# Kernel tuning notes

Measured on AMD Instinct MI355X. Metric: run time of the kernel, lower is better.

The kernel has to match this reference:

```python
import jax, jax.numpy as jnp
import numpy as np

B, S, D, H = 4, 2048, 1024, 16
DK = D // H  # d_k = d_v = 64


def setup_inputs() -> dict:
    key = jax.random.key(0)
    ks = jax.random.split(key, 9)
    sc = 0.02
    return {
        "x": jax.random.normal(ks[0], (B, S, D), dtype=jnp.float32),
        "Wq": jax.random.normal(ks[1], (H, D, DK), dtype=jnp.float32) * sc,
        "bq": jax.random.normal(ks[2], (H, DK), dtype=jnp.float32) * sc,
        "Wk": jax.random.normal(ks[3], (H, D, DK), dtype=jnp.float32) * sc,
        "bk": jax.random.normal(ks[4], (H, DK), dtype=jnp.float32) * sc,
        "Wv": jax.random.normal(ks[5], (H, D, DK), dtype=jnp.float32) * sc,
        "bv": jax.random.normal(ks[6], (H, DK), dtype=jnp.float32) * sc,
        "Wo": jax.random.normal(ks[7], (D, D), dtype=jnp.float32) * sc,
        "bo": jax.random.normal(ks[8], (D,), dtype=jnp.float32) * sc,
    }


def reference(x, Wq, bq, Wk, bk, Wv, bv, Wo, bo):
    # per-head learned projections (heads stacked on leading axis h)
    Q = jnp.einsum("bsd,hdk->bhsk", x, Wq) + bq[None, :, None, :]
    K = jnp.einsum("bsd,hdk->bhsk", x, Wk) + bk[None, :, None, :]
    V = jnp.einsum("bsd,hdk->bhsk", x, Wv) + bv[None, :, None, :]
    scores = jnp.einsum("bhsk,bhtk->bhst", Q, K) / jnp.sqrt(jnp.float32(DK))
    # causal mask: future_sight=0, past_sight=None -> positions t > s replaced by -1e9
    s_idx = jnp.arange(S)
    causal = s_idx[:, None] >= s_idx[None, :]  # [S, S] True where allowed
    scores = jnp.where(causal[None, None, :, :], scores, jnp.float32(-1e9))
    attn = jax.nn.softmax(scores, axis=-1)
    out = jnp.einsum("bhst,bhtk->bhsk", attn, V)  # [B, H, S, DK]
    # concat heads along feature dim (head order matches ModuleList order)
    cat = out.transpose(0, 2, 1, 3).reshape(B, S, D)
    return cat @ Wo + bo
```

## Files before the change

kernel.cpp:

```cpp
#include <hip/hip_runtime.h>
#include <stdint.h>

#define B_  4
#define S_  2048
#define D_  1024
#define H_  16
#define DK_ 64
#define M_  (B_ * S_)

typedef __attribute__((ext_vector_type(8))) short bf16x8;
typedef __attribute__((ext_vector_type(4))) float f32x4;

#define QSCALE 0.1803368801111204f

__device__ __forceinline__ uint16_t f2bf(float f) {
    uint32_t u = __builtin_bit_cast(uint32_t, f);
    u = (u + 0x7FFFu + ((u >> 16) & 1u)) >> 16;
    return (uint16_t)u;
}

__device__ __forceinline__ uint32_t pk2bf(float hi, float lo) {
    uint32_t a = __builtin_bit_cast(uint32_t, hi) + 0x8000u;
    uint32_t b = __builtin_bit_cast(uint32_t, lo) + 0x8000u;
    return __builtin_amdgcn_perm(a, b, 0x07060302u);
}

__global__ __launch_bounds__(256) void cvt_bf16_kernel(const float* __restrict__ in,
                                                       uint16_t* __restrict__ out, int n) {
    int i = (blockIdx.x * 256 + threadIdx.x) * 8;
    if (i >= n) return;
    float4 a = *(const float4*)&in[i];
    float4 b = *(const float4*)&in[i + 4];
    uint16_t o[8] = {f2bf(a.x), f2bf(a.y), f2bf(a.z), f2bf(a.w),
                     f2bf(b.x), f2bf(b.y), f2bf(b.z), f2bf(b.w)};
    *(uint4*)&out[i] = *(const uint4*)o;
}

__global__ __launch_bounds__(256) void transpose_cvt_kernel(
    const float* __restrict__ in, uint16_t* __restrict__ out, int R, int C) {
    __shared__ __align__(16) uint16_t tile[64][72];
    const int mat = blockIdx.z;
    const float* inm = in + (size_t)mat * R * C;
    uint16_t* outm = out + (size_t)mat * R * C;
    const int r0 = blockIdx.x * 64, c0 = blockIdx.y * 64;
    const int t = threadIdx.x;
    const int lr = t >> 2, lc = (t & 3) * 16;
    uint16_t tmp[16];
    #pragma unroll
    for (int j = 0; j < 16; j += 4) {
        float4 v = *(const float4*)&inm[(size_t)(r0 + lr) * C + c0 + lc + j];
        tmp[j] = f2bf(v.x); tmp[j + 1] = f2bf(v.y); tmp[j + 2] = f2bf(v.z); tmp[j + 3] = f2bf(v.w);
    }
    *(uint4*)&tile[lr][lc]     = ((const uint4*)tmp)[0];
    *(uint4*)&tile[lr][lc + 8] = ((const uint4*)tmp)[1];
    __syncthreads();
    const int oc = t >> 2, orr = (t & 3) * 16;
    uint16_t ot[16];
    #pragma unroll
    for (int j = 0; j < 16; ++j) ot[j] = tile[orr + j][oc];
    *(uint4*)&outm[(size_t)(c0 + oc) * R + r0 + orr]     = ((const uint4*)ot)[0];
    *(uint4*)&outm[(size_t)(c0 + oc) * R + r0 + orr + 8] = ((const uint4*)ot)[1];
}

__global__ __launch_bounds__(256) void qkv_mfma_kernel(
    const uint16_t* __restrict__ xb, const uint16_t* __restrict__ Wt,
    const float* __restrict__ bq, const float* __restrict__ bk, const float* __restrict__ bv,
    uint16_t* __restrict__ Q, uint16_t* __restrict__ K, uint16_t* __restrict__ V)
{
    __shared__ __align__(16) uint16_t As[128][72];
    __shared__ __align__(16) uint16_t Bs[128][72];
    const int tid = threadIdx.x;
    const int nb = blockIdx.x;
    const int sel = nb >> 3, npair = nb & 7;
    const int m0 = blockIdx.y * 128;
    const int lane = tid & 63, w = tid >> 6;
    const int wr = w >> 1, wc = w & 1;
    const int ll = lane & 15, quad = lane >> 4;

    const uint16_t* Bg = Wt + (size_t)nb * 128 * 1024;
    const float* bias = (sel == 0) ? bq : (sel == 1) ? bk : bv;

    const int ar = tid >> 1, ac = (tid & 1) * 32;

    f32x4 acc[4][4];
    const f32x4 zz = {0.f, 0.f, 0.f, 0.f};
    #pragma unroll
    for (int i = 0; i < 4; ++i)
        #pragma unroll
        for (int j = 0; j < 4; ++j) acc[i][j] = zz;

    for (int k0 = 0; k0 < 1024; k0 += 64) {
        __syncthreads();
        const uint16_t* ag = &xb[(size_t)(m0 + ar) * 1024 + k0 + ac];
        uint4 a0 = *(const uint4*)(ag);
        uint4 a1 = *(const uint4*)(ag + 8);
        uint4 a2 = *(const uint4*)(ag + 16);
        uint4 a3 = *(const uint4*)(ag + 24);
        const uint16_t* bg = &Bg[(size_t)ar * 1024 + k0 + ac];
        uint4 b0 = *(const uint4*)(bg);
        uint4 b1 = *(const uint4*)(bg + 8);
        uint4 b2 = *(const uint4*)(bg + 16);
        uint4 b3 = *(const uint4*)(bg + 24);
        *(uint4*)&As[ar][ac]      = a0;
        *(uint4*)&As[ar][ac + 8]  = a1;
        *(uint4*)&As[ar][ac + 16] = a2;
        *(uint4*)&As[ar][ac + 24] = a3;
        *(uint4*)&Bs[ar][ac]      = b0;
        *(uint4*)&Bs[ar][ac + 8]  = b1;
        *(uint4*)&Bs[ar][ac + 16] = b2;
        *(uint4*)&Bs[ar][ac + 24] = b3;
        __syncthreads();
        #pragma unroll
        for (int ks = 0; ks < 2; ++ks) {
            bf16x8 af[4], bfv[4];
            #pragma unroll
            for (int mt = 0; mt < 4; ++mt)
                af[mt] = *(const bf16x8*)&As[wr * 64 + mt * 16 + ll][ks * 32 + quad * 8];
            #pragma unroll
            for (int nt = 0; nt < 4; ++nt)
                bfv[nt] = *(const bf16x8*)&Bs[wc * 64 + nt * 16 + ll][ks * 32 + quad * 8];
            #pragma unroll
            for (int mt = 0; mt < 4; ++mt)
                #pragma unroll
                for (int nt = 0; nt < 4; ++nt)
                    acc[mt][nt] = __builtin_amdgcn_mfma_f32_16x16x32_bf16(af[mt], bfv[nt], acc[mt][nt], 0, 0, 0);
        }
    }

    if (sel == 2) {
        #pragma unroll
        for (int nt = 0; nt < 4; ++nt) {
            const int nl = wc * 64 + nt * 16 + ll;
            const int hh = npair * 2 + (nl >> 6);
            const int dk = nl & 63;
            const float bval = bias[npair * 128 + nl];
            #pragma unroll
            for (int mt = 0; mt < 4; ++mt) {
                int m = m0 + wr * 64 + mt * 16 + quad * 4;
                int b = m >> 11, s = m & 2047;
                uint2 pv;
                pv.x = pk2bf(acc[mt][nt][1] + bval, acc[mt][nt][0] + bval);
                pv.y = pk2bf(acc[mt][nt][3] + bval, acc[mt][nt][2] + bval);
                *(uint2*)&V[((size_t)(b * 16 + hh) * 64 + dk) * 2048 + s] = pv;
            }
        }
    } else {
        uint16_t* Out = (sel == 0) ? Q : K;
        const float qs = (sel == 0) ? QSCALE : 1.0f;
        #pragma unroll
        for (int nt = 0; nt < 4; ++nt) {
            const int nl = wc * 64 + nt * 16 + ll;
            const int hh = npair * 2 + (nl >> 6);
            const int dk = nl & 63;
            const float bval = bias[npair * 128 + nl];
            #pragma unroll
            for (int mt = 0; mt < 4; ++mt) {
                #pragma unroll
                for (int r = 0; r < 4; ++r) {
                    int m = m0 + wr * 64 + mt * 16 + quad * 4 + r;
                    int b = m >> 11, s = m & 2047;
                    float v = (acc[mt][nt][r] + bval) * qs;
                    Out[((size_t)(b * 16 + hh) * 2048 + s) * 64 + dk] = f2bf(v);
                }
            }
        }
    }
}

__global__ __launch_bounds__(256) void attn_mfma_kernel(
    const uint16_t* __restrict__ Q, const uint16_t* __restrict__ K,
    const uint16_t* __restrict__ Vg, uint16_t* __restrict__ CAT)
{
    __shared__ __align__(16) uint16_t Ks[64][72];
    __shared__ __align__(16) uint16_t Vt[64][72];
    __shared__ __align__(16) uint16_t Ps[64][72];
    __shared__ __align__(16) float rbuf[64];

    const int tid = threadIdx.x;
    const int lane = tid & 63, w = tid >> 6;
    const int ll = lane & 15, quad = lane >> 4;
    const int p = blockIdx.x;
    const int bh = blockIdx.y;
    const int b = bh >> 4, h = bh & 15;

    const uint16_t* Qbh = Q + (size_t)bh * S_ * 64;
    const uint16_t* Kbh = K + (size_t)bh * S_ * 64;
    const uint16_t* Vbh = Vg + (size_t)bh * 64 * S_;
    uint16_t* Cbh = CAT + (size_t)b * 2048 * 1024 + h * 64;

    const int sr = tid >> 2, sc = (tid & 3) * 16;

    #pragma unroll 1
    for (int phase = 0; phase < 2; ++phase) {
        const int qtb = (phase == 0) ? (31 - p) : p;
        const int q0 = qtb * 64;
        const int qw = q0 + w * 16;
        const int qg = qw + ll;

        bf16x8 qf[2];
        #pragma unroll
        for (int ks = 0; ks < 2; ++ks)
            qf[ks] = *(const bf16x8*)&Qbh[(size_t)(qw + ll) * 64 + ks * 32 + quad * 8];

        float l_run = 0.f;
        f32x4 oacc[4];
        const f32x4 zz = {0.f, 0.f, 0.f, 0.f};
        #pragma unroll
        for (int j = 0; j < 4; ++j) oacc[j] = zz;

        for (int kt = 0; kt <= qtb; ++kt) {
            const int tb = kt * 64;
            __syncthreads();
            {
                const uint16_t* g = &Kbh[(size_t)(tb + sr) * 64 + sc];
                uint4 v0 = *(const uint4*)g, v1 = *(const uint4*)(g + 8);
                *(uint4*)&Ks[sr][sc] = v0;
                *(uint4*)&Ks[sr][sc + 8] = v1;
            }
            {
                const uint16_t* g = &Vbh[(size_t)sr * 2048 + tb + sc];
                uint4 v0 = *(const uint4*)g, v1 = *(const uint4*)(g + 8);
                *(uint4*)&Vt[sr][sc] = v0;
                *(uint4*)&Vt[sr][sc + 8] = v1;
            }
            __syncthreads();

            f32x4 sacc[4];
            #pragma unroll
            for (int i = 0; i < 4; ++i) sacc[i] = zz;
            #pragma unroll
            for (int ks = 0; ks < 2; ++ks) {
                #pragma unroll
                for (int tt = 0; tt < 4; ++tt) {
                    bf16x8 kf = *(const bf16x8*)&Ks[tt * 16 + ll][ks * 32 + quad * 8];
                    sacc[tt] = __builtin_amdgcn_mfma_f32_16x16x32_bf16(kf, qf[ks], sacc[tt], 0, 0, 0);
                }
            }

            const bool needMask = (tb + 63 > qw);
            float ls = 0.f;
            #pragma unroll
            for (int tt = 0; tt < 4; ++tt) {
                #pragma unroll
                for (int r = 0; r < 4; ++r) {
                    float v = sacc[tt][r];
                    if (needMask) {
                        int tg = tb + tt * 16 + quad * 4 + r;
                        v = (tg > qg) ? -1e30f : v;
                    }
                    float pe = exp2f(v);
                    sacc[tt][r] = pe;
                    ls += pe;
                }
            }
            ls += __shfl_xor(ls, 16);
            ls += __shfl_xor(ls, 32);
            l_run += ls;
            #pragma unroll
            for (int tt = 0; tt < 4; ++tt) {
                uint2 pv;
                pv.x = pk2bf(sacc[tt][1], sacc[tt][0]);
                pv.y = pk2bf(sacc[tt][3], sacc[tt][2]);
                *(uint2*)&Ps[w * 16 + ll][tt * 16 + quad * 4] = pv;
            }
            __syncthreads();

            #pragma unroll
            for (int ks = 0; ks < 2; ++ks) {
                bf16x8 pf = *(const bf16x8*)&Ps[w * 16 + ll][ks * 32 + quad * 8];
                #pragma unroll
                for (int nt = 0; nt < 4; ++nt) {
                    bf16x8 vf = *(const bf16x8*)&Vt[nt * 16 + ll][ks * 32 + quad * 8];
                    oacc[nt] = __builtin_amdgcn_mfma_f32_16x16x32_bf16(pf, vf, oacc[nt], 0, 0, 0);
                }
            }
        }

        if (quad == 0) rbuf[w * 16 + ll] = 1.f / l_run;
        __syncthreads();
        f32x4 li = *(const f32x4*)&rbuf[w * 16 + quad * 4];
        #pragma unroll
        for (int r = 0; r < 4; ++r) {
            int q = q0 + w * 16 + quad * 4 + r;
            #pragma unroll
            for (int nt = 0; nt < 4; ++nt) {
                float v = oacc[nt][r] * li[r];
                Cbh[(size_t)q * 1024 + nt * 16 + ll] = f2bf(v);
            }
        }
        __syncthreads();
    }
}

__global__ __launch_bounds__(256) void oproj_mfma_kernel(
    const uint16_t* __restrict__ CATb, const uint16_t* __restrict__ Wot,
    const float* __restrict__ bo, float* __restrict__ out)
{
    __shared__ __align__(16) uint16_t As[128][72];
    __shared__ __align__(16) uint16_t Bs[128][72];
    const int tid = threadIdx.x;
    const int n0 = blockIdx.x * 128;
    const int m0 = blockIdx.y * 128;
    const int lane = tid & 63, w = tid >> 6;
    const int wr = w >> 1, wc = w & 1;
    const int ll = lane & 15, quad = lane >> 4;

    const int ar = tid >> 1, ac = (tid & 1) * 32;

    f32x4 acc[4][4];
    const f32x4 zz = {0.f, 0.f, 0.f, 0.f};
    #pragma unroll
    for (int i = 0; i < 4; ++i)
        #pragma unroll
        for (int j = 0; j < 4; ++j) acc[i][j] = zz;

    for (int k0 = 0; k0 < 1024; k0 += 64) {
        __syncthreads();
        const uint16_t* ag = &CATb[(size_t)(m0 + ar) * 1024 + k0 + ac];
        uint4 a0 = *(const uint4*)(ag);
        uint4 a1 = *(const uint4*)(ag + 8);
        uint4 a2 = *(const uint4*)(ag + 16);
        uint4 a3 = *(const uint4*)(ag + 24);
        const uint16_t* bg = &Wot[(size_t)(n0 + ar) * 1024 + k0 + ac];
        uint4 b0 = *(const uint4*)(bg);
        uint4 b1 = *(const uint4*)(bg + 8);
        uint4 b2 = *(const uint4*)(bg + 16);
        uint4 b3 = *(const uint4*)(bg + 24);
        *(uint4*)&As[ar][ac]      = a0;
        *(uint4*)&As[ar][ac + 8]  = a1;
        *(uint4*)&As[ar][ac + 16] = a2;
        *(uint4*)&As[ar][ac + 24] = a3;
        *(uint4*)&Bs[ar][ac]      = b0;
        *(uint4*)&Bs[ar][ac + 8]  = b1;
        *(uint4*)&Bs[ar][ac + 16] = b2;
        *(uint4*)&Bs[ar][ac + 24] = b3;
        __syncthreads();
        #pragma unroll
        for (int ks = 0; ks < 2; ++ks) {
            bf16x8 af[4], bfv[4];
            #pragma unroll
            for (int mt = 0; mt < 4; ++mt)
                af[mt] = *(const bf16x8*)&As[wr * 64 + mt * 16 + ll][ks * 32 + quad * 8];
            #pragma unroll
            for (int nt = 0; nt < 4; ++nt)
                bfv[nt] = *(const bf16x8*)&Bs[wc * 64 + nt * 16 + ll][ks * 32 + quad * 8];
            #pragma unroll
            for (int mt = 0; mt < 4; ++mt)
                #pragma unroll
                for (int nt = 0; nt < 4; ++nt)
                    acc[mt][nt] = __builtin_amdgcn_mfma_f32_16x16x32_bf16(af[mt], bfv[nt], acc[mt][nt], 0, 0, 0);
        }
    }

    #pragma unroll
    for (int nt = 0; nt < 4; ++nt) {
        const int nl = wc * 64 + nt * 16 + ll;
        const float bval = bo[n0 + nl];
        #pragma unroll
        for (int mt = 0; mt < 4; ++mt) {
            #pragma unroll
            for (int r = 0; r < 4; ++r) {
                int m = m0 + wr * 64 + mt * 16 + quad * 4 + r;
                out[(size_t)m * 1024 + n0 + nl] = acc[mt][nt][r] + bval;
            }
        }
    }
}

extern "C" void kernel_launch(void* const* d_in, const int* in_sizes, int n_in,
                              void* d_out, int out_size, void* d_ws, size_t ws_size,
                              hipStream_t stream) {
    const float* x  = (const float*)d_in[0];
    const float* Wq = (const float*)d_in[1];
    const float* bq = (const float*)d_in[2];
    const float* Wk = (const float*)d_in[3];
    const float* bk = (const float*)d_in[4];
    const float* Wv = (const float*)d_in[5];
    const float* bv = (const float*)d_in[6];
    const float* Wo = (const float*)d_in[7];
    const float* bo = (const float*)d_in[8];

    uint8_t* p = (uint8_t*)d_ws;
    uint16_t* xb   = (uint16_t*)p; p += (size_t)M_ * D_ * 2;
    uint16_t* Wt   = (uint16_t*)p; p += (size_t)3 * H_ * DK_ * D_ * 2;
    uint16_t* Wot  = (uint16_t*)p; p += (size_t)D_ * D_ * 2;
    uint16_t* Qb   = (uint16_t*)p; p += (size_t)B_ * H_ * S_ * DK_ * 2;
    uint16_t* Kb   = (uint16_t*)p; p += (size_t)B_ * H_ * S_ * DK_ * 2;
    uint16_t* Vb   = (uint16_t*)p; p += (size_t)B_ * H_ * S_ * DK_ * 2;
    uint16_t* CATb = (uint16_t*)p;

    cvt_bf16_kernel<<<dim3((M_ * D_) / 2048), 256, 0, stream>>>(x, xb, M_ * D_);
    transpose_cvt_kernel<<<dim3(D_ / 64, 1, H_), 256, 0, stream>>>(Wq, Wt, D_, DK_);
    transpose_cvt_kernel<<<dim3(D_ / 64, 1, H_), 256, 0, stream>>>(Wk, Wt + (size_t)H_ * DK_ * D_, D_, DK_);
    transpose_cvt_kernel<<<dim3(D_ / 64, 1, H_), 256, 0, stream>>>(Wv, Wt + (size_t)2 * H_ * DK_ * D_, D_, DK_);
    transpose_cvt_kernel<<<dim3(D_ / 64, D_ / 64, 1), 256, 0, stream>>>(Wo, Wot, D_, D_);

    qkv_mfma_kernel<<<dim3(24, M_ / 128), 256, 0, stream>>>(xb, Wt, bq, bk, bv, Qb, Kb, Vb);
    attn_mfma_kernel<<<dim3(16, B_ * H_), 256, 0, stream>>>(Qb, Kb, Vb, CATb);
    oproj_mfma_kernel<<<dim3(8, M_ / 128), 256, 0, stream>>>(CATb, Wot, bo, (float*)d_out);
}
```

Before: 303.1 us.

## Enlarge attention query tile to 128 rows and compute row sums via MFMA

The attention kernel now processes 128-query tiles, with each wave owning 32 rows, so every K/V tile loaded into shared memory is reused across twice as many queries. Each wave writes only its own rows of the P buffer, so the barrier between writing P and the PV MFMA is removed. Row sums are accumulated with an extra MFMA against a ones vector instead of shuffle reductions, and the hardware exp2 intrinsic is used. The three Q/K/V weight transposes are merged into one launch. In exchange the grid halves to 512 blocks, which may reduce occupancy and load balance, and per-thread register pressure rises.

Result: faster. 289.9 us (-4.4%).

```diff
diff --git a/kernel.cpp b/kernel.cpp
--- a/kernel.cpp
+++ b/kernel.cpp
@@ -36,12 +36,40 @@
     *(uint4*)&out[i] = *(const uint4*)o;
 }
 
+__global__ __launch_bounds__(256) void transpose_cvt_qkv_kernel(
+    const float* __restrict__ Wq, const float* __restrict__ Wk,
+    const float* __restrict__ Wv, uint16_t* __restrict__ Wt) {
+    __shared__ __align__(16) uint16_t tile[64][72];
+    const int z = blockIdx.z;
+    const int sel = z >> 4, mat = z & 15;
+    const float* base = (sel == 0) ? Wq : (sel == 1) ? Wk : Wv;
+    const float* inm = base + (size_t)mat * 1024 * 64;
+    uint16_t* outm = Wt + (size_t)z * 65536;
+    const int r0 = blockIdx.x * 64;
+    const int t = threadIdx.x;
+    const int lr = t >> 2, lc = (t & 3) * 16;
+    uint16_t tmp[16];
+    #pragma unroll
+    for (int j = 0; j < 16; j += 4) {
+        float4 v = *(const float4*)&inm[(size_t)(r0 + lr) * 64 + lc + j];
+        tmp[j] = f2bf(v.x); tmp[j + 1] = f2bf(v.y); tmp[j + 2] = f2bf(v.z); tmp[j + 3] = f2bf(v.w);
+    }
+    *(uint4*)&tile[lr][lc]     = ((const uint4*)tmp)[0];
+    *(uint4*)&tile[lr][lc + 8] = ((const uint4*)tmp)[1];
+    __syncthreads();
+    const int oc = t >> 2, orr = (t & 3) * 16;
+    uint16_t ot[16];
+    #pragma unroll
+    for (int j = 0; j < 16; ++j) ot[j] = tile[orr + j][oc];
+    *(uint4*)&outm[(size_t)oc * 1024 + r0 + orr]     = ((const uint4*)ot)[0];
+    *(uint4*)&outm[(size_t)oc * 1024 + r0 + orr + 8] = ((const uint4*)ot)[1];
+}
+
 __global__ __launch_bounds__(256) void transpose_cvt_kernel(
     const float* __restrict__ in, uint16_t* __restrict__ out, int R, int C) {
     __shared__ __align__(16) uint16_t tile[64][72];
-    const int mat = blockIdx.z;
-    const float* inm = in + (size_t)mat * R * C;
-    uint16_t* outm = out + (size_t)mat * R * C;
+    const float* inm = in;
+    uint16_t* outm = out;
     const int r0 = blockIdx.x * 64, c0 = blockIdx.y * 64;
     const int t = threadIdx.x;
     const int lr = t >> 2, lc = (t & 3) * 16;
@@ -173,8 +201,7 @@
 {
     __shared__ __align__(16) uint16_t Ks[64][72];
     __shared__ __align__(16) uint16_t Vt[64][72];
-    __shared__ __align__(16) uint16_t Ps[64][72];
-    __shared__ __align__(16) float rbuf[64];
+    __shared__ __align__(16) uint16_t Ps[128][72];
 
     const int tid = threadIdx.x;
     const int lane = tid & 63, w = tid >> 6;
@@ -190,25 +217,37 @@
 
     const int sr = tid >> 2, sc = (tid & 3) * 16;
 
+    bf16x8 onesf;
+    #pragma unroll
+    for (int j = 0; j < 8; ++j) onesf[j] = (ll == 0) ? (short)0x3F80 : (short)0;
+
+    const f32x4 zz = {0.f, 0.f, 0.f, 0.f};
+
     #pragma unroll 1
     for (int phase = 0; phase < 2; ++phase) {
-        const int qtb = (phase == 0) ? (31 - p) : p;
-        const int q0 = qtb * 64;
-        const int qw = q0 + w * 16;
-        const int qg = qw + ll;
-
-        bf16x8 qf[2];
-        #pragma unroll
-        for (int ks = 0; ks < 2; ++ks)
-            qf[ks] = *(const bf16x8*)&Qbh[(size_t)(qw + ll) * 64 + ks * 32 + quad * 8];
-
-        float l_run = 0.f;
-        f32x4 oacc[4];
-        const f32x4 zz = {0.f, 0.f, 0.f, 0.f};
-        #pragma unroll
-        for (int j = 0; j < 4; ++j) oacc[j] = zz;
-
-        for (int kt = 0; kt <= qtb; ++kt) {
+        const int qtb = (phase == 0) ? (15 - p) : p;
+        const int q0 = qtb * 128;
+        const int qw = q0 + w * 32;
+
+        bf16x8 qf[2][2];
+        #pragma unroll
+        for (int mt = 0; mt < 2; ++mt)
+            #pragma unroll
+            for (int ks = 0; ks < 2; ++ks)
+                qf[mt][ks] = *(const bf16x8*)&Qbh[(size_t)(qw + mt * 16 + ll) * 64 + ks * 32 + quad * 8];
+
+        f32x4 oacc[2][4];
+        f32x4 lacc[2];
+        #pragma unroll
+        for (int i = 0; i < 2; ++i) {
+            lacc[i] = zz;
+            #pragma unroll
+            for (int j = 0; j < 4; ++j) oacc[i][j] = zz;
+        }
+
+        const int ktmax = 2 * qtb + 1;
+
+        for (int kt = 0; kt <= ktmax; ++kt) {
             const int tb = kt * 64;
             __syncthreads();
             {
@@ -225,70 +264,82 @@
             }
             __syncthreads();
 
-            f32x4 sacc[4];
-            #pragma unroll
-            for (int i = 0; i < 4; ++i) sacc[i] = zz;
-            #pragma unroll
-            for (int ks = 0; ks < 2; ++ks) {
-                #pragma unroll
-                for (int tt = 0; tt < 4; ++tt) {
-                    bf16x8 kf = *(const bf16x8*)&Ks[tt * 16 + ll][ks * 32 + quad * 8];
-                    sacc[tt] = __builtin_amdgcn_mfma_f32_16x16x32_bf16(kf, qf[ks], sacc[tt], 0, 0, 0);
+            const bool active = (tb <= qw + 31);
+            if (active) {
+                f32x4 sacc[4][2];
+                #pragma unroll
+                for (int i = 0; i < 4; ++i)
+                    #pragma unroll
+                    for (int j = 0; j < 2; ++j) sacc[i][j] = zz;
+                #pragma unroll
+                for (int ks = 0; ks < 2; ++ks) {
+                    #pragma unroll
+                    for (int tt = 0; tt < 4; ++tt) {
+                        bf16x8 kf = *(const bf16x8*)&Ks[tt * 16 + ll][ks * 32 + quad * 8];
+                        #pragma unroll
+                        for (int mt = 0; mt < 2; ++mt)
+                            sacc[tt][mt] = __builtin_amdgcn_mfma_f32_16x16x32_bf16(kf, qf[mt][ks], sacc[tt][mt], 0, 0, 0);
+                    }
                 }
-            }
-
-            const bool needMask = (tb + 63 > qw);
-            float ls = 0.f;
-            #pragma unroll
-            for (int tt = 0; tt < 4; ++tt) {
-                #pragma unroll
-                for (int r = 0; r < 4; ++r) {
-                    float v = sacc[tt][r];
-                    if (needMask) {
-                        int tg = tb + tt * 16 + quad * 4 + r;
-                        v = (tg > qg) ? -1e30f : v;
+
+                const bool needMask = (tb + 63 > qw);
+                #pragma unroll
+                for (int mt = 0; mt < 2; ++mt) {
+                    const int qg = qw + mt * 16 + ll;
+                    #pragma unroll
+                    for (int tt = 0; tt < 4; ++tt) {
+                        #pragma unroll
+                        for (int r = 0; r < 4; ++r) {
+                            float v = sacc[tt][mt][r];
+                            if (needMask) {
+                                int tg = tb + tt * 16 + quad * 4 + r;
+                                v = (tg > qg) ? -1e30f : v;
+                            }
+                            sacc[tt][mt][r] = __builtin_amdgcn_exp2f(v);
+                        }
+                        uint2 pv;
+                        pv.x = pk2bf(sacc[tt][mt][1], sacc[tt][mt][0]);
+                        pv.y = pk2bf(sacc[tt][mt][3], sacc[tt][mt][2]);
+                        *(uint2*)&Ps[w * 32 + mt * 16 + ll][tt * 16 + quad * 4] = pv;
                     }
-                    float pe = exp2f(v);
-                    sacc[tt][r] = pe;
-                    ls += pe;
                 }
-            }
-            ls += __shfl_xor(ls, 16);
-            ls += __shfl_xor(ls, 32);
-            l_run += ls;
-            #pragma unroll
-            for (int tt = 0; tt < 4; ++tt) {
-                uint2 pv;
-                pv.x = pk2bf(sacc[tt][1], sacc[tt][0]);
-                pv.y = pk2bf(sacc[tt][3], sacc[tt][2]);
-                *(uint2*)&Ps[w * 16 + ll][tt * 16 + quad * 4] = pv;
-            }
-            __syncthreads();
-
-            #pragma unroll
-            for (int ks = 0; ks < 2; ++ks) {
-                bf16x8 pf = *(const bf16x8*)&Ps[w * 16 + ll][ks * 32 + quad * 8];
+
+                #pragma unroll
+                for (int ks = 0; ks < 2; ++ks) {
+                    bf16x8 pf[2], vf[4];
+                    #pragma unroll
+                    for (int mt = 0; mt < 2; ++mt)
+                        pf[mt] = *(const bf16x8*)&Ps[w * 32 + mt * 16 + ll][ks * 32 + quad * 8];
+                    #pragma unroll
+                    for (int nt = 0; nt < 4; ++nt)
+                        vf[nt] = *(const bf16x8*)&Vt[nt * 16 + ll][ks * 32 + quad * 8];
+                    #pragma unroll
+                    for (int mt = 0; mt < 2; ++mt) {
+                        lacc[mt] = __builtin_amdgcn_mfma_f32_16x16x32_bf16(pf[mt], onesf, lacc[mt], 0, 0, 0);
+                        #pragma unroll
+                        for (int nt = 0; nt < 4; ++nt)
+                            oacc[mt][nt] = __builtin_amdgcn_mfma_f32_16x16x32_bf16(pf[mt], vf[nt], oacc[mt][nt], 0, 0, 0);
+                    }
+                }
+            }
+        }
+
+        #pragma unroll
+        for (int mt = 0; mt < 2; ++mt) {
+            f32x4 li;
+            #pragma unroll
+            for (int r = 0; r < 4; ++r)
+                li[r] = 1.0f / __shfl(lacc[mt][r], lane & 48);
+            #pragma unroll
+            for (int r = 0; r < 4; ++r) {
+                int q = qw + mt * 16 + quad * 4 + r;
                 #pragma unroll
                 for (int nt = 0; nt < 4; ++nt) {
-                    bf16x8 vf = *(const bf16x8*)&Vt[nt * 16 + ll][ks * 32 + quad * 8];
-                    oacc[nt] = __builtin_amdgcn_mfma_f32_16x16x32_bf16(pf, vf, oacc[nt], 0, 0, 0);
+                    float v = oacc[mt][nt][r] * li[r];
+                    Cbh[(size_t)q * 1024 + nt * 16 + ll] = f2bf(v);
                 }
             }
         }
-
-        if (quad == 0) rbuf[w * 16 + ll] = 1.f / l_run;
-        __syncthreads();
-        f32x4 li = *(const f32x4*)&rbuf[w * 16 + quad * 4];
-        #pragma unroll
-        for (int r = 0; r < 4; ++r) {
-            int q = q0 + w * 16 + quad * 4 + r;
-            #pragma unroll
-            for (int nt = 0; nt < 4; ++nt) {
-                float v = oacc[nt][r] * li[r];
-                Cbh[(size_t)q * 1024 + nt * 16 + ll] = f2bf(v);
-            }
-        }
-        __syncthreads();
     }
 }
 
@@ -390,12 +441,10 @@
     uint16_t* CATb = (uint16_t*)p;
 
     cvt_bf16_kernel<<<dim3((M_ * D_) / 2048), 256, 0, stream>>>(x, xb, M_ * D_);
-    transpose_cvt_kernel<<<dim3(D_ / 64, 1, H_), 256, 0, stream>>>(Wq, Wt, D_, DK_);
-    transpose_cvt_kernel<<<dim3(D_ / 64, 1, H_), 256, 0, stream>>>(Wk, Wt + (size_t)H_ * DK_ * D_, D_, DK_);
-    transpose_cvt_kernel<<<dim3(D_ / 64, 1, H_), 256, 0, stream>>>(Wv, Wt + (size_t)2 * H_ * DK_ * D_, D_, DK_);
+    transpose_cvt_qkv_kernel<<<dim3(16, 1, 48), 256, 0, stream>>>(Wq, Wk, Wv, Wt);
     transpose_cvt_kernel<<<dim3(D_ / 64, D_ / 64, 1), 256, 0, stream>>>(Wo, Wot, D_, D_);
 
     qkv_mfma_kernel<<<dim3(24, M_ / 128), 256, 0, stream>>>(xb, Wt, bq, bk, bv, Qb, Kb, Vb);
-    attn_mfma_kernel<<<dim3(16, B_ * H_), 256, 0, stream>>>(Qb, Kb, Vb, CATb);
+    attn_mfma_kernel<<<dim3(8, B_ * H_), 256, 0, stream>>>(Qb, Kb, Vb, CATb);
     oproj_mfma_kernel<<<dim3(8, M_ / 128), 256, 0, stream>>>(CATb, Wot, bo, (float*)d_out);
 }
```
